# Kernel optimization log

Hardware: AMD Instinct MI355X
Metric: run time of the kernel (lower is better)

Reference implementation:

```python
import jax, jax.numpy as jnp
import numpy as np

# module config (matches init_kwargs)
NUM_COL_HEADS = 4
NUM_ROW_HEADS = 4
EMBED_COL_DIM = 64
EMBED_ROW_DIM = 64
HEAD_COL = EMBED_COL_DIM // NUM_COL_HEADS  # 16
HEAD_ROW = EMBED_ROW_DIM // NUM_ROW_HEADS  # 16
SCALE = (HEAD_COL * HEAD_ROW) ** (-0.5)


def matrix_mul(x, u, v):
    # 'nm,blnd,dk->blmk'
    return jnp.einsum('nm,blnd,dk->blmk', u, x, v)


def setup_inputs() -> dict:
    key = jax.random.key(0)
    k1, k2, k3, k4, k5 = jax.random.split(key, 5)
    B, L, C, R = 2, 2048, 64, 64
    x = jax.random.normal(k1, (B, L, C, R), dtype=jnp.float32)
    qkv_u = jax.random.uniform(k2, (C, EMBED_COL_DIM), dtype=jnp.float32)
    qkv_v = jax.random.uniform(k3, (R, EMBED_ROW_DIM * 3), dtype=jnp.float32)
    proj_u = jax.random.uniform(k4, (EMBED_COL_DIM, C), dtype=jnp.float32)
    proj_v = jax.random.uniform(k5, (EMBED_ROW_DIM, R), dtype=jnp.float32)
    return {"x": x, "qkv_u": qkv_u, "qkv_v": qkv_v, "proj_u": proj_u, "proj_v": proj_v}


def reference(x, qkv_u, qkv_v, proj_u, proj_v):
    B, L, C, R = x.shape
    # bilinear QKV projection: [B,L,embed_col,3*embed_row]
    qkv = matrix_mul(x, qkv_u, qkv_v)
    qkv = qkv.reshape(B, L, 3, NUM_COL_HEADS, HEAD_COL, NUM_ROW_HEADS, HEAD_ROW)
    qkv = qkv.transpose(2, 0, 3, 5, 1, 4, 6)  # [3,B,Mc,Mr,L,Hc,Hw]
    q, k, v = qkv[0], qkv[1], qkv[2]
    # attention over combined (head_col, head_row) feature axes
    attn = jnp.einsum('bmnihw,bmnjhw->bmnij', q, k)
    attn = jax.nn.softmax(attn / SCALE, axis=-1)  # note: divides by scale, as in source
    out = jnp.einsum('bmnij,bmnjhw->bmnihw', attn, v)
    out = out.transpose(0, 3, 1, 4, 2, 5).reshape(B, L, EMBED_COL_DIM, EMBED_ROW_DIM)
    out = matrix_mul(out, proj_u, proj_v)
    return out
```

## Files before the change

### kernel.cpp

```cpp
#include <hip/hip_runtime.h>
#include <hip/hip_fp16.h>

typedef _Float16 f16x8 __attribute__((ext_vector_type(8)));
typedef _Float16 f16x4 __attribute__((ext_vector_type(4)));
typedef float f32x4 __attribute__((ext_vector_type(4)));


__device__ __forceinline__ void stage16(const _Float16* g, _Float16* l) {
  __builtin_amdgcn_global_load_lds(
      (const __attribute__((address_space(1))) void*)g,
      (__attribute__((address_space(3))) void*)l, 16, 0, 0);
}

__device__ __forceinline__ unsigned int pk2(float a, float b) {
  union { _Float16 h[2]; unsigned int u; } x;
  x.h[0] = (_Float16)a; x.h[1] = (_Float16)b;
  return x.u;
}

struct hl16 { _Float16 h, l; };
__device__ __forceinline__ hl16 split_f16(float v) {
  hl16 r;
  r.h = (_Float16)v;
  r.l = (_Float16)(v - (float)r.h);
  return r;
}

__global__ __launch_bounds__(256) void qkv_kernel(
    const float* __restrict__ x, const float* __restrict__ u,
    const float* __restrict__ v, _Float16* __restrict__ Q,
    _Float16* __restrict__ K, _Float16* __restrict__ V) {
  __shared__ _Float16 sm[24576];
  _Float16* xs_hi = sm;
  _Float16* xs_lo = sm + 4096;
  _Float16* us_hi = sm + 8192;
  _Float16* us_lo = sm + 12288;
  _Float16* Ts_hi = sm + 16384;
  _Float16* Ts_lo = sm + 20480;
  _Float16* vc_hi = sm;
  _Float16* vc_lo = sm + 7680;
  _Float16* qk16 = sm;
  const int bl = blockIdx.x;
  const int b = bl >> 11, l = bl & 2047;
  const int t = threadIdx.x;
  const int w = t >> 6, lane = t & 63;
  const int l15 = lane & 15, quad = lane >> 4;

  {
    const int d = t & 63, wq = t >> 6;
#pragma unroll
    for (int rr = 0; rr < 2; ++rr) {
      const int n0 = wq * 8 + rr * 32;
      f16x8 xh, xl, uh, ul;
#pragma unroll
      for (int j = 0; j < 8; ++j) {
        hl16 sx = split_f16(x[((size_t)bl << 12) + (n0 + j) * 64 + d]);
        hl16 su = split_f16(u[(n0 + j) * 64 + d]);
        xh[j] = sx.h; xl[j] = sx.l;
        uh[j] = su.h; ul[j] = su.l;
      }
      const int un = ((n0 >> 3) ^ (d & 7)) << 3;
      *(f16x8*)(xs_hi + (d << 6) + un) = xh;
      *(f16x8*)(xs_lo + (d << 6) + un) = xl;
      *(f16x8*)(us_hi + (d << 6) + un) = uh;
      *(f16x8*)(us_lo + (d << 6) + un) = ul;
    }
  }
  __syncthreads();

  {
    f32x4 dacc[4];
#pragma unroll
    for (int mt = 0; mt < 4; ++mt) dacc[mt] = (f32x4){0.f, 0.f, 0.f, 0.f};
    const int d = (w << 4) | l15;
#pragma unroll
    for (int ks = 0; ks < 2; ++ks) {
      const int ug = (((ks * 4 + quad) ^ (d & 7)) << 3);
      f16x8 bh = *(const f16x8*)(xs_hi + (d << 6) + ug);
      f16x8 blo = *(const f16x8*)(xs_lo + (d << 6) + ug);
#pragma unroll
      for (int mt = 0; mt < 4; ++mt) {
        const int m = (mt << 4) | l15;
        const int um = (((ks * 4 + quad) ^ (m & 7)) << 3);
        f16x8 ah = *(const f16x8*)(us_hi + (m << 6) + um);
        f16x8 al = *(const f16x8*)(us_lo + (m << 6) + um);
        dacc[mt] = __builtin_amdgcn_mfma_f32_16x16x32_f16(ah, bh, dacc[mt], 0, 0, 0);
        dacc[mt] = __builtin_amdgcn_mfma_f32_16x16x32_f16(ah, blo, dacc[mt], 0, 0, 0);
        dacc[mt] = __builtin_amdgcn_mfma_f32_16x16x32_f16(al, bh, dacc[mt], 0, 0, 0);
      }
    }
#pragma unroll
    for (int mt = 0; mt < 4; ++mt) {
#pragma unroll
      for (int r = 0; r < 4; ++r) {
        const int m = (mt << 4) | (quad << 2) | r;
        const int dd = (w << 4) | l15;
        const int off = (m << 6) + ((((dd >> 3) ^ (m & 7)) << 3) | (dd & 7));
        hl16 st = split_f16(dacc[mt][r]);
        Ts_hi[off] = st.h;
        Ts_lo[off] = st.l;
      }
    }
  }
  __syncthreads();

  f32x4 cacc[4][3];
#pragma unroll
  for (int mt = 0; mt < 4; ++mt)
#pragma unroll
    for (int kt = 0; kt < 3; ++kt) cacc[mt][kt] = (f32x4){0.f, 0.f, 0.f, 0.f};

  for (int chk = 0; chk < 2; ++chk) {
#pragma unroll
    for (int rr = 0; rr < 3; ++rr) {
      const int c768 = t + 256 * rr;
      const int k = c768 >> 2, sg = c768 & 3;
      f16x8 vh, vl;
#pragma unroll
      for (int j = 0; j < 8; ++j) {
        hl16 sv = split_f16(v[(chk * 32 + sg * 8 + j) * 192 + k]);
        vh[j] = sv.h; vl[j] = sv.l;
      }
      *(f16x8*)(vc_hi + k * 40 + sg * 8) = vh;
      *(f16x8*)(vc_lo + k * 40 + sg * 8) = vl;
    }
    __syncthreads();
    f16x8 ah[4], al[4];
#pragma unroll
    for (int mt = 0; mt < 4; ++mt) {
      const int m = (mt << 4) | l15;
      const int off = (m << 6) + (((chk * 4 + quad) ^ (m & 7)) << 3);
      ah[mt] = *(const f16x8*)(Ts_hi + off);
      al[mt] = *(const f16x8*)(Ts_lo + off);
    }
#pragma unroll
    for (int kt = 0; kt < 3; ++kt) {
      const int k = w * 48 + kt * 16 + l15;
      f16x8 bh = *(const f16x8*)(vc_hi + k * 40 + quad * 8);
      f16x8 blo = *(const f16x8*)(vc_lo + k * 40 + quad * 8);
#pragma unroll
      for (int mt = 0; mt < 4; ++mt) {
        cacc[mt][kt] = __builtin_amdgcn_mfma_f32_16x16x32_f16(ah[mt], bh, cacc[mt][kt], 0, 0, 0);
        cacc[mt][kt] = __builtin_amdgcn_mfma_f32_16x16x32_f16(ah[mt], blo, cacc[mt][kt], 0, 0, 0);
        cacc[mt][kt] = __builtin_amdgcn_mfma_f32_16x16x32_f16(al[mt], bh, cacc[mt][kt], 0, 0, 0);
      }
    }
    __syncthreads();
  }

#pragma unroll
  for (int mt = 0; mt < 4; ++mt)
#pragma unroll
    for (int kt = 0; kt < 3; ++kt) {
      const int k = w * 48 + kt * 16 + l15;
#pragma unroll
      for (int r = 0; r < 4; ++r) {
        const int m = (mt << 4) | (quad << 2) | r;
        qk16[m * 192 + k] = (_Float16)cacc[mt][kt][r];
      }
    }
  __syncthreads();

#pragma unroll
  for (int s = 0; s < 3; ++s) {
    const int rho = t + 256 * s;
    const int m = rho / 12, rem = rho - m * 12;
    const int k64 = rem >> 2, mr = rem & 3;
    const int chf = 3 * m + k64;
    const int t3 = chf >> 6, ch = chf & 63;
    const int f0 = (ch & 15) << 4;
    const int h = (b << 4) | ((ch >> 4) << 2) | mr;
    const _Float16* src = qk16 + m * 192 + k64 * 64 + mr * 16;
    f16x8 a0 = *(const f16x8*)src;
    f16x8 a1 = *(const f16x8*)(src + 8);
    _Float16* base = (t3 == 0) ? Q : (t3 == 1) ? K : V;
    _Float16* dst = base + (((size_t)h * 2048 + l) << 8) + f0;
    *(f16x8*)dst = a0;
    *(f16x8*)(dst + 8) = a1;
  }
}

__global__ __launch_bounds__(256) void vtrans_kernel(
    const _Float16* __restrict__ V, _Float16* __restrict__ Vt) {
  __shared__ _Float16 tb[64 * 72];
  const int bid = blockIdx.x;
  const int h = bid >> 7;
  const int lt = (bid >> 2) & 31;
  const int ft = bid & 3;
  const int l0 = lt << 6, f0 = ft << 6;
  const int t = threadIdx.x;
  const int r = t >> 2, s = (t & 3) << 4;
  const _Float16* src = V + (((size_t)h * 2048 + l0 + r) << 8) + f0 + s;
  *(f16x8*)(tb + r * 72 + s) = *(const f16x8*)src;
  *(f16x8*)(tb + r * 72 + s + 8) = *(const f16x8*)(src + 8);
  __syncthreads();
  _Float16 buf[16];
#pragma unroll
  for (int j = 0; j < 16; ++j) buf[j] = tb[(s + j) * 72 + r];
  _Float16* dst = Vt + (((size_t)(h << 8) + f0 + r) << 11) + l0 + s;
  *(f16x8*)dst = *(f16x8*)buf;
  *(f16x8*)(dst + 8) = *(f16x8*)(buf + 8);
}

__global__ __launch_bounds__(256, 2) void attn_kernel(
    const _Float16* __restrict__ Q, const _Float16* __restrict__ K,
    const _Float16* __restrict__ Vt, _Float16* __restrict__ O) {
  __shared__ _Float16 Ks[2][32 * 256];
  __shared__ _Float16 Vs[2][256 * 32];
  __shared__ unsigned int Ps[4 * 32 * 18];
  const int i = blockIdx.x;
  const int h = (i & 7) * 4 + (i >> 7);
  const int qt = (i >> 3) & 15;
  const int tid = threadIdx.x;
  const int w = tid >> 6, lane = tid & 63;
  const int l15 = lane & 15, quad = lane >> 4;
  const int q0 = qt * 128 + w * 32;

  const _Float16* Kt = K + (((size_t)h * 2048) << 8);
  const _Float16* Vtb = Vt + (((size_t)h << 8) << 11);

  f16x8 qf[2][8];
#pragma unroll
  for (int qh = 0; qh < 2; ++qh) {
    const _Float16* qb = Q + (((size_t)h * 2048 + q0 + qh * 16 + l15) << 8) + quad * 8;
#pragma unroll
    for (int kc = 0; kc < 8; ++kc) qf[qh][kc] = *(const f16x8*)(qb + kc * 32);
  }

  f32x4 oacc[2][16];
#pragma unroll
  for (int qh = 0; qh < 2; ++qh)
#pragma unroll
    for (int fb = 0; fb < 16; ++fb) oacc[qh][fb] = (f32x4){0.f, 0.f, 0.f, 0.f};
  float m2[2] = {-1e30f, -1e30f};
  float ell[2] = {0.f, 0.f};
  const float SC = 23.083120654223414f;

  auto stage_tile = [&](int kt, int bb) {
    const int k0 = kt * 32;
#pragma unroll
    for (int o = 0; o < 4; ++o) {
      const int c = tid + o * 256;
      const int row = c >> 5, unit = c & 31;
      stage16(Kt + (((size_t)(k0 + row)) << 8) + ((unit ^ (row & 7)) << 3),
              &Ks[bb][c * 8]);
      const int g = c >> 3, ip = c & 7;
      const int sl = (g << 3) | (ip ^ (g & 7));
      const int f = sl >> 2, ku = sl & 3;
      stage16(Vtb + (((size_t)f) << 11) + k0 + ku * 8, &Vs[bb][c * 8]);
    }
  };

  unsigned int* pw = Ps + w * 32 * 18;
  stage_tile(0, 0);
  for (int kt = 0; kt < 64; ++kt) {
    const int cb = kt & 1;
    if (kt < 63) {
      stage_tile(kt + 1, cb ^ 1);
      asm volatile("s_waitcnt vmcnt(8)" ::: "memory");
    } else {
      asm volatile("s_waitcnt vmcnt(0)" ::: "memory");
    }
    __builtin_amdgcn_s_barrier();
    asm volatile("" ::: "memory");

    f32x4 c00 = {0.f, 0.f, 0.f, 0.f}, c01 = c00, c10 = c00, c11 = c00;
#pragma unroll
    for (int kc = 0; kc < 8; ++kc) {
      const int u0 = ((kc * 4 + quad) ^ (l15 & 7)) << 3;
      f16x8 kf0 = *(const f16x8*)(&Ks[cb][l15 * 256 + u0]);
      f16x8 kf1 = *(const f16x8*)(&Ks[cb][(16 + l15) * 256 + u0]);
      c00 = __builtin_amdgcn_mfma_f32_16x16x32_f16(kf0, qf[0][kc], c00, 0, 0, 0);
      c01 = __builtin_amdgcn_mfma_f32_16x16x32_f16(kf0, qf[1][kc], c01, 0, 0, 0);
      c10 = __builtin_amdgcn_mfma_f32_16x16x32_f16(kf1, qf[0][kc], c10, 0, 0, 0);
      c11 = __builtin_amdgcn_mfma_f32_16x16x32_f16(kf1, qf[1][kc], c11, 0, 0, 0);
    }

    float alpha[2];
    bool upd = false;
#pragma unroll
    for (int qh = 0; qh < 2; ++qh) {
      const f32x4 ck0 = qh ? c01 : c00;
      const f32x4 ck1 = qh ? c11 : c10;
      float s0[4], s1[4];
#pragma unroll
      for (int r = 0; r < 4; ++r) { s0[r] = ck0[r] * SC; s1[r] = ck1[r] * SC; }
      float mx = fmaxf(fmaxf(fmaxf(s0[0], s0[1]), fmaxf(s0[2], s0[3])),
                       fmaxf(fmaxf(s1[0], s1[1]), fmaxf(s1[2], s1[3])));
      mx = fmaxf(mx, __shfl_xor(mx, 16));
      mx = fmaxf(mx, __shfl_xor(mx, 32));
      const float mo = m2[qh];
      const bool u8 = (mx > mo + 8.f);
      const float mn = u8 ? mx : mo;
      m2[qh] = mn;
      upd |= u8;
      const float a = exp2f(mo - mn);
      alpha[qh] = a;
      float p0[4], p1[4];
#pragma unroll
      for (int r = 0; r < 4; ++r) { p0[r] = exp2f(s0[r] - mn); p1[r] = exp2f(s1[r] - mn); }
      ell[qh] = ell[qh] * a + ((p0[0] + p0[1]) + (p0[2] + p0[3])) +
                ((p1[0] + p1[1]) + (p1[2] + p1[3]));
      unsigned int* row = pw + (qh * 16 + l15) * 18;
      row[quad * 2 + 0] = pk2(p0[0], p0[1]);
      row[quad * 2 + 1] = pk2(p0[2], p0[3]);
      row[8 + quad * 2 + 0] = pk2(p1[0], p1[1]);
      row[8 + quad * 2 + 1] = pk2(p1[2], p1[3]);
    }
    if (__any(upd)) {
#pragma unroll
      for (int qh = 0; qh < 2; ++qh)
#pragma unroll
        for (int fb = 0; fb < 16; ++fb) oacc[qh][fb] *= alpha[qh];
    }
    f16x8 pf[2];
#pragma unroll
    for (int qh = 0; qh < 2; ++qh) {
      const _Float16* pr = (const _Float16*)(pw + (qh * 16 + l15) * 18);
      union { f16x8 v; f16x4 h[2]; } tmp;
      tmp.h[0] = *(const f16x4*)(pr + quad * 8);
      tmp.h[1] = *(const f16x4*)(pr + quad * 8 + 4);
      pf[qh] = tmp.v;
    }
#pragma unroll
    for (int fb = 0; fb < 16; ++fb) {
      const int f = fb * 16 + l15;
      const int g = f >> 1;
      const int ip = (((f & 1) << 2) | quad) ^ (g & 7);
      f16x8 vf = *(const f16x8*)(&Vs[cb][(((g << 3) | ip)) * 8]);
      oacc[0][fb] = __builtin_amdgcn_mfma_f32_16x16x32_f16(vf, pf[0], oacc[0][fb], 0, 0, 0);
      oacc[1][fb] = __builtin_amdgcn_mfma_f32_16x16x32_f16(vf, pf[1], oacc[1][fb], 0, 0, 0);
    }
    asm volatile("" ::: "memory");
    __builtin_amdgcn_s_barrier();
  }

#pragma unroll
  for (int qh = 0; qh < 2; ++qh) {
    float e = ell[qh];
    e += __shfl_xor(e, 16);
    e += __shfl_xor(e, 32);
    const float inv = 1.f / e;
    _Float16* ob = O + (((size_t)h * 2048 + q0 + qh * 16 + l15) << 8) + quad * 4;
#pragma unroll
    for (int fb = 0; fb < 16; ++fb) {
      f16x4 ov;
#pragma unroll
      for (int r = 0; r < 4; ++r) ov[r] = (_Float16)(oacc[qh][fb][r] * inv);
      *(f16x4*)(ob + fb * 16) = ov;
    }
  }
}

__global__ __launch_bounds__(256) void proj_kernel(
    const _Float16* __restrict__ O, const float* __restrict__ pu,
    const float* __restrict__ pv, float* __restrict__ out) {
  __shared__ float os[4096];
  __shared__ float pus[4096];
  __shared__ float tmps[4096];
  const int bl = blockIdx.x;
  const int b = bl >> 11, l = bl & 2047;
  const int t = threadIdx.x;
#pragma unroll
  for (int i = 0; i < 4; ++i)
    ((float4*)pus)[t + 256 * i] = ((const float4*)pu)[t + 256 * i];
  {
    const int hh = t >> 4, hc = t & 15;
    const int mc = hh >> 2, mr = hh & 3;
    const int hg = (b << 4) | hh;
    const _Float16* src = O + (((size_t)hg * 2048 + l) << 8) + hc * 16;
    float* dst = os + (mc * 16 + hc) * 64 + mr * 16;
    f16x8 v0 = *(const f16x8*)(src);
    f16x8 v1 = *(const f16x8*)(src + 8);
#pragma unroll
    for (int j = 0; j < 8; ++j) {
      dst[j] = (float)v0[j];
      dst[8 + j] = (float)v1[j];
    }
  }
  __syncthreads();
  {
    const int m0 = (t >> 4) << 2, d0 = (t & 15) << 2;
    float acc[4][4] = {};
    for (int n = 0; n < 64; ++n) {
      float uv[4], xv[4];
      *(float4*)uv = *(const float4*)&pus[n * 64 + m0];
      *(float4*)xv = *(const float4*)&os[n * 64 + d0];
#pragma unroll
      for (int i = 0; i < 4; ++i)
#pragma unroll
        for (int j = 0; j < 4; ++j) acc[i][j] += uv[i] * xv[j];
    }
    __syncthreads();
#pragma unroll
    for (int i = 0; i < 4; ++i)
#pragma unroll
      for (int j = 0; j < 4; ++j) tmps[(d0 + j) * 64 + m0 + i] = acc[i][j];
  }
#pragma unroll
  for (int i = 0; i < 4; ++i)
    ((float4*)os)[t + 256 * i] = ((const float4*)pv)[t + 256 * i];
  __syncthreads();
  {
    const int m0 = (t >> 4) << 2, k0 = (t & 15) << 2;
    float acc[4][4] = {};
    for (int d = 0; d < 64; ++d) {
      float tv[4], vv[4];
      *(float4*)tv = *(const float4*)&tmps[d * 64 + m0];
      *(float4*)vv = *(const float4*)&os[d * 64 + k0];
#pragma unroll
      for (int i = 0; i < 4; ++i)
#pragma unroll
        for (int j = 0; j < 4; ++j) acc[i][j] += tv[i] * vv[j];
    }
    float* og = out + ((size_t)bl << 12);
#pragma unroll
    for (int i = 0; i < 4; ++i) {
      float4 r;
      r.x = acc[i][0]; r.y = acc[i][1]; r.z = acc[i][2]; r.w = acc[i][3];
      *(float4*)&og[(m0 + i) * 64 + k0] = r;
    }
  }
}

extern "C" void kernel_launch(void* const* d_in, const int* in_sizes, int n_in,
                              void* d_out, int out_size, void* d_ws, size_t ws_size,
                              hipStream_t stream) {
  (void)in_sizes; (void)n_in; (void)out_size; (void)ws_size;
  const float* x = (const float*)d_in[0];
  const float* u = (const float*)d_in[1];
  const float* v = (const float*)d_in[2];
  const float* pu = (const float*)d_in[3];
  const float* pv = (const float*)d_in[4];
  const size_t SEG = (size_t)32 * 2048 * 256;
  _Float16* Q = (_Float16*)d_ws;
  _Float16* K = Q + SEG;
  _Float16* Vt = K + SEG;
  _Float16* O = Vt + SEG;
  _Float16* V = O;
  qkv_kernel<<<4096, 256, 0, stream>>>(x, u, v, Q, K, V);
  vtrans_kernel<<<4096, 256, 0, stream>>>(V, Vt);
  attn_kernel<<<512, 256, 0, stream>>>(Q, K, Vt, O);
  proj_kernel<<<4096, 256, 0, stream>>>(O, pu, pv, (float*)d_out);
}
```

Before: 452.0 us.

## Move output projection to MFMA with split-f16 precision and swizzled LDS

Rewrites proj_kernel so its two 64x64 bilinear matmuls run on f16 MFMA instructions instead of scalar FP32 FMAs. The weights and the intermediate product are split into high and low f16 parts, so extra MFMAs recover near-FP32 accuracy. LDS holds f16 data in an XOR-swizzled layout to avoid bank conflicts. The weight split is recomputed in every block, and the output writes become scalar, strided stores instead of float4 stores.

```diff
diff --git a/kernel.cpp b/kernel.cpp
--- a/kernel.cpp
+++ b/kernel.cpp
@@ -355,70 +355,119 @@
 __global__ __launch_bounds__(256) void proj_kernel(
     const _Float16* __restrict__ O, const float* __restrict__ pu,
     const float* __restrict__ pv, float* __restrict__ out) {
-  __shared__ float os[4096];
-  __shared__ float pus[4096];
-  __shared__ float tmps[4096];
+  __shared__ _Float16 sm[20480];
+  _Float16* os = sm;
+  _Float16* put_hi = sm + 4096;
+  _Float16* put_lo = sm + 8192;
+  _Float16* pvt_hi = sm + 12288;
+  _Float16* pvt_lo = sm + 16384;
+  _Float16* gt_hi = sm;
+  _Float16* gt_lo = sm + 12288;
   const int bl = blockIdx.x;
   const int b = bl >> 11, l = bl & 2047;
   const int t = threadIdx.x;
-#pragma unroll
-  for (int i = 0; i < 4; ++i)
-    ((float4*)pus)[t + 256 * i] = ((const float4*)pu)[t + 256 * i];
+  const int w = t >> 6, lane = t & 63;
+  const int l15 = lane & 15, quad = lane >> 4;
+
   {
     const int hh = t >> 4, hc = t & 15;
     const int mc = hh >> 2, mr = hh & 3;
     const int hg = (b << 4) | hh;
     const _Float16* src = O + (((size_t)hg * 2048 + l) << 8) + hc * 16;
-    float* dst = os + (mc * 16 + hc) * 64 + mr * 16;
+    const int n = mc * 16 + hc, d0 = mr * 16;
     f16x8 v0 = *(const f16x8*)(src);
     f16x8 v1 = *(const f16x8*)(src + 8);
-#pragma unroll
-    for (int j = 0; j < 8; ++j) {
-      dst[j] = (float)v0[j];
-      dst[8 + j] = (float)v1[j];
-    }
-  }
-  __syncthreads();
-  {
-    const int m0 = (t >> 4) << 2, d0 = (t & 15) << 2;
-    float acc[4][4] = {};
-    for (int n = 0; n < 64; ++n) {
-      float uv[4], xv[4];
-      *(float4*)uv = *(const float4*)&pus[n * 64 + m0];
-      *(float4*)xv = *(const float4*)&os[n * 64 + d0];
-#pragma unroll
-      for (int i = 0; i < 4; ++i)
-#pragma unroll
-        for (int j = 0; j < 4; ++j) acc[i][j] += uv[i] * xv[j];
-    }
-    __syncthreads();
-#pragma unroll
-    for (int i = 0; i < 4; ++i)
-#pragma unroll
-      for (int j = 0; j < 4; ++j) tmps[(d0 + j) * 64 + m0 + i] = acc[i][j];
-  }
-#pragma unroll
-  for (int i = 0; i < 4; ++i)
-    ((float4*)os)[t + 256 * i] = ((const float4*)pv)[t + 256 * i];
-  __syncthreads();
-  {
-    const int m0 = (t >> 4) << 2, k0 = (t & 15) << 2;
-    float acc[4][4] = {};
-    for (int d = 0; d < 64; ++d) {
-      float tv[4], vv[4];
-      *(float4*)tv = *(const float4*)&tmps[d * 64 + m0];
-      *(float4*)vv = *(const float4*)&os[d * 64 + k0];
-#pragma unroll
-      for (int i = 0; i < 4; ++i)
-#pragma unroll
-        for (int j = 0; j < 4; ++j) acc[i][j] += tv[i] * vv[j];
+    *(f16x8*)(os + (n << 6) + ((((d0 >> 3) + 0) ^ (n & 7)) << 3)) = v0;
+    *(f16x8*)(os + (n << 6) + ((((d0 >> 3) + 1) ^ (n & 7)) << 3)) = v1;
+  }
+  {
+    const int c = t & 63, wq = t >> 6;
+#pragma unroll
+    for (int rr = 0; rr < 2; ++rr) {
+      const int r0 = wq * 8 + rr * 32;
+      f16x8 uh, ul, vh, vl;
+#pragma unroll
+      for (int j = 0; j < 8; ++j) {
+        hl16 su = split_f16(pu[(r0 + j) * 64 + c]);
+        hl16 sv = split_f16(pv[(r0 + j) * 64 + c]);
+        uh[j] = su.h; ul[j] = su.l;
+        vh[j] = sv.h; vl[j] = sv.l;
+      }
+      const int un = ((r0 >> 3) ^ (c & 7)) << 3;
+      *(f16x8*)(put_hi + (c << 6) + un) = uh;
+      *(f16x8*)(put_lo + (c << 6) + un) = ul;
+      *(f16x8*)(pvt_hi + (c << 6) + un) = vh;
+      *(f16x8*)(pvt_lo + (c << 6) + un) = vl;
+    }
+  }
+  __syncthreads();
+
+  f32x4 gacc[4];
+#pragma unroll
+  for (int nt = 0; nt < 4; ++nt) gacc[nt] = (f32x4){0.f, 0.f, 0.f, 0.f};
+  {
+    const int k = (w << 4) | l15;
+#pragma unroll
+    for (int ks = 0; ks < 2; ++ks) {
+      const int uk = (((ks * 4 + quad) ^ (k & 7)) << 3);
+      f16x8 bh = *(const f16x8*)(pvt_hi + (k << 6) + uk);
+      f16x8 blo = *(const f16x8*)(pvt_lo + (k << 6) + uk);
+#pragma unroll
+      for (int nt = 0; nt < 4; ++nt) {
+        const int n = (nt << 4) | l15;
+        const int un = (((ks * 4 + quad) ^ (n & 7)) << 3);
+        f16x8 a = *(const f16x8*)(os + (n << 6) + un);
+        gacc[nt] = __builtin_amdgcn_mfma_f32_16x16x32_f16(a, bh, gacc[nt], 0, 0, 0);
+        gacc[nt] = __builtin_amdgcn_mfma_f32_16x16x32_f16(a, blo, gacc[nt], 0, 0, 0);
+      }
+    }
+  }
+  __syncthreads();
+  {
+    const int k = (w << 4) | l15;
+#pragma unroll
+    for (int nt = 0; nt < 4; ++nt) {
+#pragma unroll
+      for (int r = 0; r < 4; ++r) {
+        const int n = (nt << 4) | (quad << 2) | r;
+        const int off = (k << 6) + ((((n >> 3) ^ (k & 7)) << 3) | (n & 7));
+        hl16 sg = split_f16(gacc[nt][r]);
+        gt_hi[off] = sg.h;
+        gt_lo[off] = sg.l;
+      }
+    }
+  }
+  __syncthreads();
+
+  {
+    f32x4 cacc[4];
+#pragma unroll
+    for (int mt = 0; mt < 4; ++mt) cacc[mt] = (f32x4){0.f, 0.f, 0.f, 0.f};
+    const int k = (w << 4) | l15;
+#pragma unroll
+    for (int ks = 0; ks < 2; ++ks) {
+      const int uk = (((ks * 4 + quad) ^ (k & 7)) << 3);
+      f16x8 bh = *(const f16x8*)(gt_hi + (k << 6) + uk);
+      f16x8 blo = *(const f16x8*)(gt_lo + (k << 6) + uk);
+#pragma unroll
+      for (int mt = 0; mt < 4; ++mt) {
+        const int m = (mt << 4) | l15;
+        const int um = (((ks * 4 + quad) ^ (m & 7)) << 3);
+        f16x8 ah = *(const f16x8*)(put_hi + (m << 6) + um);
+        f16x8 al = *(const f16x8*)(put_lo + (m << 6) + um);
+        cacc[mt] = __builtin_amdgcn_mfma_f32_16x16x32_f16(ah, bh, cacc[mt], 0, 0, 0);
+        cacc[mt] = __builtin_amdgcn_mfma_f32_16x16x32_f16(ah, blo, cacc[mt], 0, 0, 0);
+        cacc[mt] = __builtin_amdgcn_mfma_f32_16x16x32_f16(al, bh, cacc[mt], 0, 0, 0);
+      }
     }
     float* og = out + ((size_t)bl << 12);
 #pragma unroll
-    for (int i = 0; i < 4; ++i) {
-      float4 r;
-      r.x = acc[i][0]; r.y = acc[i][1]; r.z = acc[i][2]; r.w = acc[i][3];
-      *(float4*)&og[(m0 + i) * 64 + k0] = r;
+    for (int mt = 0; mt < 4; ++mt) {
+#pragma unroll
+      for (int r = 0; r < 4; ++r) {
+        const int m = (mt << 4) | (quad << 2) | r;
+        og[m * 64 + k] = cacc[mt][r];
+      }
     }
   }
 }
```

After: 420.1 us. -7.1%, faster.
